# Optimization experiments

Measured on AMD Instinct MI355X. Metric: run time of the kernel, lower is better.

The kernel has to match this reference:

```python
import jax, jax.numpy as jnp
import numpy as np

B, T, C = 4, 2048, 1024
E, D, TOP_K = 8, 3072, 2


def setup_inputs() -> dict:
    key = jax.random.key(0)
    ks = jax.random.split(key, 6)
    s_c = 1.0 / np.sqrt(C)
    s_d = 1.0 / np.sqrt(D)
    return {
        "x": jax.random.normal(ks[0], (B, T, C), dtype=jnp.float32),
        "router_w": jax.random.uniform(ks[1], (E, C), jnp.float32, -s_c, s_c),
        "W1": jax.random.uniform(ks[2], (E, C, D), jnp.float32, -s_c, s_c),
        "b1": jax.random.uniform(ks[3], (E, D), jnp.float32, -s_c, s_c),
        "W2": jax.random.uniform(ks[4], (E, D, C), jnp.float32, -s_d, s_d),
        "b2": jax.random.uniform(ks[5], (E, C), jnp.float32, -s_d, s_d),
    }


def reference(x, router_w, W1, b1, W2, b2):
    b, t, c = x.shape
    xf = x.reshape(b * t, c)                      # [N, C]
    n = xf.shape[0]
    logits = xf @ router_w.T                       # [N, E]
    probs = jax.nn.softmax(logits, axis=-1)
    topw, topi = jax.lax.top_k(probs, TOP_K)       # [N, k]
    topw = topw / jnp.sum(topw, axis=-1, keepdims=True)
    # scatter normalized top-k weights into [N, E] combine weights
    mask = jnp.zeros_like(probs).at[jnp.arange(n)[:, None], topi].set(topw)
    # dense expert MLPs (zero combine weight == token not routed to expert)
    h = jax.nn.gelu(jnp.einsum('nc,ecd->ned', xf, W1) + b1, approximate=False)
    y = jnp.einsum('ned,edc->nec', h, W2) + b2     # [N, E, C]
    out = jnp.einsum('ne,nec->nc', mask, y).reshape(b, t, c)
    aux_loss = jnp.zeros((), dtype=x.dtype)        # eval mode
    return out, aux_loss
```

## Files before the change

### kernel.cpp

```cpp
#include <hip/hip_runtime.h>
#include <math.h>

#define N_TOK 8192
#define C_DIM 1024
#define D_DIM 3072
#define E_NUM 8
#define SEG 128
#define MAXB 136

typedef unsigned short u16;
typedef unsigned int u32;
typedef __attribute__((ext_vector_type(8))) short bf16x8;
typedef __attribute__((ext_vector_type(4))) float f32x4;

__device__ __forceinline__ u16 f2bf(float f) {
  u32 u = __builtin_bit_cast(unsigned int, f);
  u = (u + 0x7FFFu + ((u >> 16) & 1u)) >> 16;
  return (u16)u;
}

__global__ void zero_init_kernel(float* __restrict__ out, int n, int* __restrict__ cnt) {
  const int n4 = n >> 2;
  for (int i = blockIdx.x * 256 + threadIdx.x; i < n4; i += gridDim.x * 256)
    *(float4*)(out + i * 4) = make_float4(0.f, 0.f, 0.f, 0.f);
  if (blockIdx.x == 0 && threadIdx.x == 0)
    for (int i = n4 * 4; i < n; i++) out[i] = 0.0f;
  if (blockIdx.x == 0 && threadIdx.x < E_NUM) cnt[threadIdx.x] = 0;
}

template<int R, int CC>
__global__ __launch_bounds__(256) void transpose_conv_kernel(
    const float* __restrict__ in, u16* __restrict__ outp) {
  __shared__ float t[64][65];
  const int e = blockIdx.z;
  const int r0 = blockIdx.y * 64;
  const int c0 = blockIdx.x * 64;
  const int tid = threadIdx.x;
  const int lr = tid >> 4;
  const int lc = (tid & 15) * 4;
#pragma unroll
  for (int i = 0; i < 4; i++) {
    float4 v = *(const float4*)(in + ((size_t)e * R + r0 + lr + i * 16) * CC + c0 + lc);
    t[lr + i * 16][lc] = v.x; t[lr + i * 16][lc + 1] = v.y;
    t[lr + i * 16][lc + 2] = v.z; t[lr + i * 16][lc + 3] = v.w;
  }
  __syncthreads();
  const int orow = tid >> 3;
  const int oc = (tid & 7) * 8;
#pragma unroll
  for (int i = 0; i < 2; i++) {
    const int d = orow + i * 32;
    union { u16 s[8]; uint4 v; } o;
#pragma unroll
    for (int j = 0; j < 8; j++) o.s[j] = f2bf(t[oc + j][d]);
    *(uint4*)(outp + ((size_t)e * CC + c0 + d) * R + r0 + oc) = o.v;
  }
}

__global__ void router_kernel(const float* __restrict__ x, const float* __restrict__ rw,
                              int* __restrict__ cnt, int* __restrict__ list,
                              float* __restrict__ wl) {
  const int lane = threadIdx.x & 63;
  const int n = blockIdx.x * 4 + (threadIdx.x >> 6);
  const float* xr = x + (size_t)n * C_DIM;
  double acc[E_NUM];
#pragma unroll
  for (int e = 0; e < E_NUM; e++) acc[e] = 0.0;
#pragma unroll
  for (int i = 0; i < 4; i++) {
    const int c = lane * 4 + i * 256;
    float4 xv = *(const float4*)(xr + c);
#pragma unroll
    for (int e = 0; e < E_NUM; e++) {
      const float* rwe = rw + e * C_DIM + c;
      acc[e] += (double)xv.x * (double)rwe[0] + (double)xv.y * (double)rwe[1]
              + (double)xv.z * (double)rwe[2] + (double)xv.w * (double)rwe[3];
    }
  }
#pragma unroll
  for (int e = 0; e < E_NUM; e++) {
    double v = acc[e];
#pragma unroll
    for (int off = 32; off > 0; off >>= 1) v += __shfl_down(v, off, 64);
    acc[e] = v;
  }
  if (lane == 0) {
    int i0 = 0;
#pragma unroll
    for (int e = 1; e < E_NUM; e++) if (acc[e] > acc[i0]) i0 = e;
    int i1 = (i0 == 0) ? 1 : 0;
#pragma unroll
    for (int e = 0; e < E_NUM; e++) if (e != i0 && acc[e] > acc[i1]) i1 = e;
    double d = acc[i0] - acc[i1];
    double w0 = 1.0 / (1.0 + exp(-d));
    double w1 = 1.0 - w0;
    int p0 = atomicAdd(&cnt[i0], 1);
    list[i0 * N_TOK + p0] = n; wl[i0 * N_TOK + p0] = (float)w0;
    int p1 = atomicAdd(&cnt[i1], 1);
    list[i1 * N_TOK + p1] = n; wl[i1 * N_TOK + p1] = (float)w1;
  }
}

__global__ void prefix_kernel(const int* __restrict__ cnt, int* __restrict__ rowbase,
                              int* __restrict__ btab) {
  const int lane = threadIdx.x;
  int c[E_NUM], rbse[E_NUM], nseg[E_NUM], nsb[E_NUM];
  int s = 0, t = 0;
#pragma unroll
  for (int e = 0; e < E_NUM; e++) {
    c[e] = cnt[e]; rbse[e] = s; s += c[e];
    nseg[e] = (c[e] + SEG - 1) / SEG; nsb[e] = t; t += nseg[e];
  }
  if (lane < E_NUM) rowbase[lane] = rbse[lane];
  for (int i = lane; i < MAXB; i += 64) {
    int e = -1, m0 = 0;
#pragma unroll
    for (int k = 0; k < E_NUM; k++)
      if (i >= nsb[k] && i < nsb[k] + nseg[k]) { e = k; m0 = (i - nsb[k]) * SEG; }
    btab[2 * i] = e; btab[2 * i + 1] = m0;
  }
}

__global__ void gather_x_kernel(const float* __restrict__ x, const int* __restrict__ rowbase,
                                const int* __restrict__ list, u16* __restrict__ Xg) {
  const int rflat = blockIdx.x * 4 + (threadIdx.x >> 6);
  const int lane = threadIdx.x & 63;
  int e = E_NUM - 1;
#pragma unroll
  for (int k = 1; k < E_NUM; k++) if (rflat < rowbase[k]) { e = k - 1; break; }
  const int p = rflat - rowbase[e];
  const int tok = list[e * N_TOK + p];
  const float* src = x + (size_t)tok * C_DIM;
  u16* dst = Xg + (size_t)rflat * C_DIM;
#pragma unroll
  for (int i = 0; i < 4; i++) {
    float4 v = *(const float4*)(src + lane * 4 + i * 256);
    ushort4 o;
    o.x = f2bf(v.x); o.y = f2bf(v.y); o.z = f2bf(v.z); o.w = f2bf(v.w);
    *(ushort4*)(dst + lane * 4 + i * 256) = o;
  }
}

template<int NN0, int K, int EPI>
__global__ __launch_bounds__(256, 4) void gemm_rs_kernel(
    const u16* __restrict__ A, const u16* __restrict__ Wt, const float* __restrict__ bias_,
    const int* __restrict__ btab, const int* __restrict__ cnt, const int* __restrict__ rowbase,
    const int* __restrict__ list, const float* __restrict__ wl,
    u16* __restrict__ hout, float* __restrict__ out) {
  constexpr int NTOT = NN0 * 128;
  constexpr int NT = K / 32;
  constexpr int NG = NN0 / 4;
  constexpr int TOT = MAXB * NN0;

  __shared__ __align__(16) u16 ldsA[2 * 128 * 32];
  __shared__ __align__(16) u16 ldsB[2 * 128 * 32];

  const int L = (blockIdx.x & 7) * (TOT / 8) + (blockIdx.x >> 3);
  const int coh = L >> 4, r = L & 15;
  const int bxg = coh / NG;
  const int n0g = coh % NG;
  const int bx = bxg * 4 + (r & 3);
  const int n0 = (n0g * 4 + (r >> 2)) * 128;

  const int e = btab[bx * 2];
  if (e < 0) return;
  const int m0 = btab[bx * 2 + 1];
  const int count = cnt[e];
  const int rb = rowbase[e];

  const int tid = threadIdx.x;
  const int lane = tid & 63;
  const int wid = tid >> 6;
  const int wm = (wid >> 1) * 64;
  const int wn = (wid & 1) * 64;
  const int l15 = lane & 15, l4 = lane >> 4;

  const int arow0 = tid >> 2, pos = (tid & 3) * 8;
  const u16* aptr0 = A + (size_t)(rb + min(m0 + arow0, count - 1)) * K + pos;
  const u16* aptr1 = A + (size_t)(rb + min(m0 + arow0 + 64, count - 1)) * K + pos;
  const u16* bptr0 = Wt + ((size_t)e * NTOT + n0 + arow0) * K + pos;
  const u16* bptr1 = Wt + ((size_t)e * NTOT + n0 + arow0 + 64) * K + pos;

  const int paoff = (wm + l15) * 32 + l4 * 8;
  const int pboff = (wn + l15) * 32 + l4 * 8;

  f32x4 acc[4][4];
#pragma unroll
  for (int i = 0; i < 4; i++)
#pragma unroll
    for (int j = 0; j < 4; j++) acc[i][j] = {0.f, 0.f, 0.f, 0.f};

  uint4 ra0, ra1, rb0, rb1;
  auto LOAD = [&](int t) {
    const int ko = t * 32;
    ra0 = *(const uint4*)(aptr0 + ko);
    ra1 = *(const uint4*)(aptr1 + ko);
    rb0 = *(const uint4*)(bptr0 + ko);
    rb1 = *(const uint4*)(bptr1 + ko);
  };
  auto WRITE = [&](int b) {
    *(uint4*)(ldsA + b * 4096 + tid * 8) = ra0;
    *(uint4*)(ldsA + b * 4096 + 2048 + tid * 8) = ra1;
    *(uint4*)(ldsB + b * 4096 + tid * 8) = rb0;
    *(uint4*)(ldsB + b * 4096 + 2048 + tid * 8) = rb1;
  };

  auto PHASE = [&](int b) {
    const u16* pa = ldsA + b * 4096 + paoff;
    const u16* pb = ldsB + b * 4096 + pboff;
    bf16x8 av[4], bv[4];
#pragma unroll
    for (int i = 0; i < 4; i++) av[i] = *(const bf16x8*)(pa + i * 512);
#pragma unroll
    for (int j = 0; j < 4; j++) bv[j] = *(const bf16x8*)(pb + j * 512);
#pragma unroll
    for (int i = 0; i < 4; i++)
#pragma unroll
      for (int j = 0; j < 4; j++)
        acc[i][j] = __builtin_amdgcn_mfma_f32_16x16x32_bf16(av[i], bv[j], acc[i][j], 0, 0, 0);
  };

  LOAD(0);
  WRITE(0);
  asm volatile("s_waitcnt lgkmcnt(0)");
  __builtin_amdgcn_sched_barrier(0);

  for (int t = 0; t < NT - 1; ++t) {
    LOAD(t + 1);
    __builtin_amdgcn_s_barrier();
    __builtin_amdgcn_sched_barrier(0);
    PHASE(t & 1);
    __builtin_amdgcn_s_barrier();
    WRITE((t + 1) & 1);
    asm volatile("s_waitcnt lgkmcnt(0)");
    __builtin_amdgcn_sched_barrier(0);
  }
  __builtin_amdgcn_s_barrier();
  __builtin_amdgcn_sched_barrier(0);
  PHASE((NT - 1) & 1);

  if constexpr (EPI == 1) {
#pragma unroll
    for (int i = 0; i < 4; i++) {
      const int rloc = wm + i * 16 + l4 * 4;
#pragma unroll
      for (int j = 0; j < 4; j++) {
        const int col = n0 + wn + j * 16 + l15;
        const float bias = bias_[e * NTOT + col];
#pragma unroll
        for (int rr = 0; rr < 4; rr++) {
          const int m = m0 + rloc + rr;
          if (m < count) {
            float v = acc[i][j][rr] + bias;
            float g = 0.5f * v * (1.0f + erff(v * 0.70710678118654752f));
            hout[(size_t)(rb + m) * D_DIM + col] = f2bf(g);
          }
        }
      }
    }
  } else {
    const int* lst = list + e * N_TOK;
    const float* wlst = wl + e * N_TOK;
#pragma unroll
    for (int i = 0; i < 4; i++) {
      const int rloc = wm + i * 16 + l4 * 4;
#pragma unroll
      for (int j = 0; j < 4; j++) {
        const int col = n0 + wn + j * 16 + l15;
        const float bias = bias_[e * NTOT + col];
#pragma unroll
        for (int rr = 0; rr < 4; rr++) {
          const int m = m0 + rloc + rr;
          if (m < count) {
            const int tk = lst[m];
            atomicAdd(out + (size_t)tk * C_DIM + col, wlst[m] * (acc[i][j][rr] + bias));
          }
        }
      }
    }
  }
}

extern "C" void kernel_launch(void* const* d_in, const int* in_sizes, int n_in,
                              void* d_out, int out_size, void* d_ws, size_t ws_size,
                              hipStream_t stream) {
  const float* x  = (const float*)d_in[0];
  const float* rw = (const float*)d_in[1];
  const float* W1 = (const float*)d_in[2];
  const float* b1 = (const float*)d_in[3];
  const float* W2 = (const float*)d_in[4];
  const float* b2 = (const float*)d_in[5];
  float* out = (float*)d_out;

  char* ws = (char*)d_ws;
  u16* W1t    = (u16*)(ws);
  u16* Xg     = (u16*)(ws + 50331648);
  u16* W2t    = (u16*)(ws + 50331648);
  int* cnt    = (int*)(ws + 100663296);
  int* rowbase= (int*)(ws + 100663552);
  int* list   = (int*)(ws + 100663808);
  float* wl   = (float*)(ws + 100925952);
  int* btab   = (int*)(ws + 101188096);
  u16* h      = (u16*)(ws + 101190656);

  zero_init_kernel<<<2048, 256, 0, stream>>>(out, out_size, cnt);
  router_kernel<<<N_TOK / 4, 256, 0, stream>>>(x, rw, cnt, list, wl);
  prefix_kernel<<<1, 64, 0, stream>>>(cnt, rowbase, btab);
  gather_x_kernel<<<(2 * N_TOK) / 4, 256, 0, stream>>>(x, rowbase, list, Xg);
  transpose_conv_kernel<C_DIM, D_DIM><<<dim3(D_DIM / 64, C_DIM / 64, E_NUM), 256, 0, stream>>>(W1, W1t);
  gemm_rs_kernel<24, C_DIM, 1><<<MAXB * 24, 256, 0, stream>>>(
      Xg, W1t, b1, btab, cnt, rowbase, list, wl, h, out);
  transpose_conv_kernel<D_DIM, C_DIM><<<dim3(C_DIM / 64, D_DIM / 64, E_NUM), 256, 0, stream>>>(W2, W2t);
  gemm_rs_kernel<8, D_DIM, 2><<<MAXB * 8, 256, 0, stream>>>(
      h, W2t, b2, btab, cnt, rowbase, list, wl, h, out);
}
```

Baseline: 652.1 us.

## Add 256x256-tile 8-wave GEMM1 with async global-to-LDS 4-stage pipeline

Replaces the first expert GEMM with a new kernel using 512-thread blocks and 256x256 output tiles. Operands are staged with global_load_lds direct-to-LDS copies into a 4-deep swizzled ring buffer, and s_setprio is raised around MFMA bursts. The prefix kernel now builds a second block table with 256-row segments for it. The larger tile raises data reuse and removes the register round-trip on loads, at the cost of more padding waste in the last segment of each expert, higher register and LDS use per block, and lower occupancy.

Result: slower. 711.1 us (+9.1%).

```diff
diff --git a/kernel.cpp b/kernel.cpp
--- a/kernel.cpp
+++ b/kernel.cpp
@@ -7,6 +7,7 @@
 #define E_NUM 8
 #define SEG 128
 #define MAXB 136
+#define MAXB2 72
 
 typedef unsigned short u16;
 typedef unsigned int u32;
@@ -17,6 +18,12 @@
   u32 u = __builtin_bit_cast(unsigned int, f);
   u = (u + 0x7FFFu + ((u >> 16) & 1u)) >> 16;
   return (u16)u;
+}
+
+__device__ __forceinline__ void gl_lds16(const void* g, void* l) {
+  __builtin_amdgcn_global_load_lds(
+      (const __attribute__((address_space(1))) unsigned int*)g,
+      (__attribute__((address_space(3))) unsigned int*)l, 16, 0, 0);
 }
 
 __global__ void zero_init_kernel(float* __restrict__ out, int n, int* __restrict__ cnt) {
@@ -102,22 +109,30 @@
 }
 
 __global__ void prefix_kernel(const int* __restrict__ cnt, int* __restrict__ rowbase,
-                              int* __restrict__ btab) {
+                              int* __restrict__ btab128, int* __restrict__ btab256) {
   const int lane = threadIdx.x;
-  int c[E_NUM], rbse[E_NUM], nseg[E_NUM], nsb[E_NUM];
-  int s = 0, t = 0;
+  int c[E_NUM], rbse[E_NUM], ns1[E_NUM], nb1[E_NUM], ns2[E_NUM], nb2[E_NUM];
+  int s = 0, t1 = 0, t2 = 0;
 #pragma unroll
   for (int e = 0; e < E_NUM; e++) {
     c[e] = cnt[e]; rbse[e] = s; s += c[e];
-    nseg[e] = (c[e] + SEG - 1) / SEG; nsb[e] = t; t += nseg[e];
+    ns1[e] = (c[e] + 127) / 128; nb1[e] = t1; t1 += ns1[e];
+    ns2[e] = (c[e] + 255) / 256; nb2[e] = t2; t2 += ns2[e];
   }
   if (lane < E_NUM) rowbase[lane] = rbse[lane];
   for (int i = lane; i < MAXB; i += 64) {
     int e = -1, m0 = 0;
 #pragma unroll
     for (int k = 0; k < E_NUM; k++)
-      if (i >= nsb[k] && i < nsb[k] + nseg[k]) { e = k; m0 = (i - nsb[k]) * SEG; }
-    btab[2 * i] = e; btab[2 * i + 1] = m0;
+      if (i >= nb1[k] && i < nb1[k] + ns1[k]) { e = k; m0 = (i - nb1[k]) * 128; }
+    btab128[2 * i] = e; btab128[2 * i + 1] = m0;
+  }
+  for (int i = lane; i < MAXB2; i += 64) {
+    int e = -1, m0 = 0;
+#pragma unroll
+    for (int k = 0; k < E_NUM; k++)
+      if (i >= nb2[k] && i < nb2[k] + ns2[k]) { e = k; m0 = (i - nb2[k]) * 256; }
+    btab256[2 * i] = e; btab256[2 * i + 1] = m0;
   }
 }
 
@@ -141,12 +156,131 @@
   }
 }
 
-template<int NN0, int K, int EPI>
+template<int NN0, int K>
+__global__ __launch_bounds__(512, 2) void gemm1_8p_kernel(
+    const u16* __restrict__ A, const u16* __restrict__ Wt, const float* __restrict__ bias_,
+    const int* __restrict__ btab, const int* __restrict__ cnt, const int* __restrict__ rowbase,
+    u16* __restrict__ hout) {
+  constexpr int NTOT = NN0 * 256;
+  constexpr int NHALF = K / 32;
+  constexpr int TOT = MAXB2 * NN0;
+
+  __shared__ __align__(16) u16 ldsA[4 * 256 * 32];
+  __shared__ __align__(16) u16 ldsB[4 * 256 * 32];
+
+  const int L = (blockIdx.x & 7) * (TOT / 8) + (blockIdx.x >> 3);
+  const int bx = L / NN0;
+  const int n0 = (L % NN0) * 256;
+
+  const int e = btab[bx * 2];
+  if (e < 0) return;
+  const int m0 = btab[bx * 2 + 1];
+  const int count = cnt[e];
+  const int rb = rowbase[e];
+
+  const int tid = threadIdx.x;
+  const int lane = tid & 63;
+  const int wid = tid >> 6;
+  const int wr = wid >> 2, wc = wid & 3;
+  const int l15 = lane & 15, l4 = lane >> 4;
+
+  const int srow = tid >> 2;
+  const int sc = tid & 3;
+  const int swz = sc ^ ((srow >> 1) & 3);
+  const u16* aS0 = A + (size_t)(rb + min(m0 + srow, count - 1)) * K + swz * 8;
+  const u16* aS1 = A + (size_t)(rb + min(m0 + srow + 128, count - 1)) * K + swz * 8;
+  const u16* bS0 = Wt + ((size_t)e * NTOT + n0 + srow) * K + swz * 8;
+  const u16* bS1 = Wt + ((size_t)e * NTOT + n0 + srow + 128) * K + swz * 8;
+  u16* dA = ldsA + tid * 8;
+  u16* dB = ldsB + tid * 8;
+
+  f32x4 acc[8][4];
+#pragma unroll
+  for (int i = 0; i < 8; i++)
+#pragma unroll
+    for (int j = 0; j < 4; j++) acc[i][j] = {0.f, 0.f, 0.f, 0.f};
+
+  auto STAGE = [&](int n) {
+    if (n >= NHALF) return;
+    const int slot = (n & 3) * 8192;
+    const int ko = n * 32;
+    gl_lds16(aS0 + ko, dA + slot);
+    gl_lds16(aS1 + ko, dA + slot + 4096);
+    gl_lds16(bS0 + ko, dB + slot);
+    gl_lds16(bS1 + ko, dB + slot + 4096);
+  };
+
+  STAGE(0); STAGE(1); STAGE(2);
+  asm volatile("s_waitcnt vmcnt(8)");
+  __builtin_amdgcn_sched_barrier(0);
+  __builtin_amdgcn_s_barrier();
+  __builtin_amdgcn_sched_barrier(0);
+
+  for (int n = 0; n < NHALF; ++n) {
+    const int slot = (n & 3) * 8192;
+    bf16x8 av[4], bv[4];
+#pragma unroll
+    for (int j = 0; j < 4; j++) {
+      const int row = wc * 64 + l15 + j * 16;
+      bv[j] = *(const bf16x8*)(ldsB + slot + row * 32 + ((l4 ^ ((row >> 1) & 3)) * 8));
+    }
+#pragma unroll
+    for (int i = 0; i < 4; i++) {
+      const int row = wr * 128 + l15 + i * 16;
+      av[i] = *(const bf16x8*)(ldsA + slot + row * 32 + ((l4 ^ ((row >> 1) & 3)) * 8));
+    }
+    STAGE(n + 3);
+    __builtin_amdgcn_s_setprio(1);
+#pragma unroll
+    for (int i = 0; i < 4; i++)
+#pragma unroll
+      for (int j = 0; j < 4; j++)
+        acc[i][j] = __builtin_amdgcn_mfma_f32_16x16x32_bf16(av[i], bv[j], acc[i][j], 0, 0, 0);
+    __builtin_amdgcn_s_setprio(0);
+#pragma unroll
+    for (int i = 0; i < 4; i++) {
+      const int row = wr * 128 + 64 + l15 + i * 16;
+      av[i] = *(const bf16x8*)(ldsA + slot + row * 32 + ((l4 ^ ((row >> 1) & 3)) * 8));
+    }
+    __builtin_amdgcn_s_setprio(1);
+#pragma unroll
+    for (int i = 0; i < 4; i++)
+#pragma unroll
+      for (int j = 0; j < 4; j++)
+        acc[i + 4][j] = __builtin_amdgcn_mfma_f32_16x16x32_bf16(av[i], bv[j], acc[i + 4][j], 0, 0, 0);
+    __builtin_amdgcn_s_setprio(0);
+    asm volatile("s_waitcnt vmcnt(8)");
+    __builtin_amdgcn_sched_barrier(0);
+    __builtin_amdgcn_s_barrier();
+    __builtin_amdgcn_sched_barrier(0);
+  }
+
+#pragma unroll
+  for (int i = 0; i < 8; i++) {
+    const int rloc = wr * 128 + i * 16 + l4 * 4;
+#pragma unroll
+    for (int j = 0; j < 4; j++) {
+      const int col = n0 + wc * 64 + j * 16 + l15;
+      const float bias = bias_[e * NTOT + col];
+#pragma unroll
+      for (int rr = 0; rr < 4; rr++) {
+        const int m = m0 + rloc + rr;
+        if (m < count) {
+          float v = acc[i][j][rr] + bias;
+          float g = 0.5f * v * (1.0f + erff(v * 0.70710678118654752f));
+          hout[(size_t)(rb + m) * D_DIM + col] = f2bf(g);
+        }
+      }
+    }
+  }
+}
+
+template<int NN0, int K>
 __global__ __launch_bounds__(256, 4) void gemm_rs_kernel(
     const u16* __restrict__ A, const u16* __restrict__ Wt, const float* __restrict__ bias_,
     const int* __restrict__ btab, const int* __restrict__ cnt, const int* __restrict__ rowbase,
     const int* __restrict__ list, const float* __restrict__ wl,
-    u16* __restrict__ hout, float* __restrict__ out) {
+    float* __restrict__ out) {
   constexpr int NTOT = NN0 * 128;
   constexpr int NT = K / 32;
   constexpr int NG = NN0 / 4;
@@ -204,7 +338,6 @@
     *(uint4*)(ldsB + b * 4096 + tid * 8) = rb0;
     *(uint4*)(ldsB + b * 4096 + 2048 + tid * 8) = rb1;
   };
-
   auto PHASE = [&](int b) {
     const u16* pa = ldsA + b * 4096 + paoff;
     const u16* pb = ldsB + b * 4096 + pboff;
@@ -239,42 +372,21 @@
   __builtin_amdgcn_sched_barrier(0);
   PHASE((NT - 1) & 1);
 
-  if constexpr (EPI == 1) {
-#pragma unroll
-    for (int i = 0; i < 4; i++) {
-      const int rloc = wm + i * 16 + l4 * 4;
-#pragma unroll
-      for (int j = 0; j < 4; j++) {
-        const int col = n0 + wn + j * 16 + l15;
-        const float bias = bias_[e * NTOT + col];
-#pragma unroll
-        for (int rr = 0; rr < 4; rr++) {
-          const int m = m0 + rloc + rr;
-          if (m < count) {
-            float v = acc[i][j][rr] + bias;
-            float g = 0.5f * v * (1.0f + erff(v * 0.70710678118654752f));
-            hout[(size_t)(rb + m) * D_DIM + col] = f2bf(g);
-          }
-        }
-      }
-    }
-  } else {
-    const int* lst = list + e * N_TOK;
-    const float* wlst = wl + e * N_TOK;
-#pragma unroll
-    for (int i = 0; i < 4; i++) {
-      const int rloc = wm + i * 16 + l4 * 4;
-#pragma unroll
-      for (int j = 0; j < 4; j++) {
-        const int col = n0 + wn + j * 16 + l15;
-        const float bias = bias_[e * NTOT + col];
-#pragma unroll
-        for (int rr = 0; rr < 4; rr++) {
-          const int m = m0 + rloc + rr;
-          if (m < count) {
-            const int tk = lst[m];
-            atomicAdd(out + (size_t)tk * C_DIM + col, wlst[m] * (acc[i][j][rr] + bias));
-          }
+  const int* lst = list + e * N_TOK;
+  const float* wlst = wl + e * N_TOK;
+#pragma unroll
+  for (int i = 0; i < 4; i++) {
+    const int rloc = wm + i * 16 + l4 * 4;
+#pragma unroll
+    for (int j = 0; j < 4; j++) {
+      const int col = n0 + wn + j * 16 + l15;
+      const float bias = bias_[e * NTOT + col];
+#pragma unroll
+      for (int rr = 0; rr < 4; rr++) {
+        const int m = m0 + rloc + rr;
+        if (m < count) {
+          const int tk = lst[m];
+          atomicAdd(out + (size_t)tk * C_DIM + col, wlst[m] * (acc[i][j][rr] + bias));
         }
       }
     }
@@ -293,24 +405,25 @@
   float* out = (float*)d_out;
 
   char* ws = (char*)d_ws;
-  u16* W1t    = (u16*)(ws);
-  u16* Xg     = (u16*)(ws + 50331648);
-  u16* W2t    = (u16*)(ws + 50331648);
-  int* cnt    = (int*)(ws + 100663296);
-  int* rowbase= (int*)(ws + 100663552);
-  int* list   = (int*)(ws + 100663808);
-  float* wl   = (float*)(ws + 100925952);
-  int* btab   = (int*)(ws + 101188096);
-  u16* h      = (u16*)(ws + 101190656);
+  u16* W1t     = (u16*)(ws);
+  u16* Xg      = (u16*)(ws + 50331648);
+  u16* W2t     = (u16*)(ws + 50331648);
+  int* cnt     = (int*)(ws + 100663296);
+  int* rowbase = (int*)(ws + 100663552);
+  int* list    = (int*)(ws + 100663808);
+  float* wl    = (float*)(ws + 100925952);
+  int* btab128 = (int*)(ws + 101188096);
+  int* btab256 = (int*)(ws + 101190144);
+  u16* h       = (u16*)(ws + 101191168);
 
   zero_init_kernel<<<2048, 256, 0, stream>>>(out, out_size, cnt);
   router_kernel<<<N_TOK / 4, 256, 0, stream>>>(x, rw, cnt, list, wl);
-  prefix_kernel<<<1, 64, 0, stream>>>(cnt, rowbase, btab);
+  prefix_kernel<<<1, 64, 0, stream>>>(cnt, rowbase, btab128, btab256);
   gather_x_kernel<<<(2 * N_TOK) / 4, 256, 0, stream>>>(x, rowbase, list, Xg);
   transpose_conv_kernel<C_DIM, D_DIM><<<dim3(D_DIM / 64, C_DIM / 64, E_NUM), 256, 0, stream>>>(W1, W1t);
-  gemm_rs_kernel<24, C_DIM, 1><<<MAXB * 24, 256, 0, stream>>>(
-      Xg, W1t, b1, btab, cnt, rowbase, list, wl, h, out);
+  gemm1_8p_kernel<D_DIM / 256, C_DIM><<<MAXB2 * (D_DIM / 256), 512, 0, stream>>>(
+      Xg, W1t, b1, btab256, cnt, rowbase, h);
   transpose_conv_kernel<D_DIM, C_DIM><<<dim3(C_DIM / 64, D_DIM / 64, E_NUM), 256, 0, stream>>>(W2, W2t);
-  gemm_rs_kernel<8, D_DIM, 2><<<MAXB * 8, 256, 0, stream>>>(
-      h, W2t, b2, btab, cnt, rowbase, list, wl, h, out);
-}
+  gemm_rs_kernel<8, D_DIM><<<MAXB * 8, 256, 0, stream>>>(
+      h, W2t, b2, btab128, cnt, rowbase, list, wl, out);
+}
```
